# Performance work log

Hardware: AMD Instinct MI355X
Metric: run time of the kernel (lower is better)

The kernel has to match this reference:

```python
import jax, jax.numpy as jnp
import numpy as np

B = 16384
STATE = 524   # state_dim / output_size
IENC = 256    # INet output dim
ZD = 32       # z_dim
H = 256       # expert hidden size
E = 5         # num_experts
HG = 256      # gating hidden size
IN1 = STATE + IENC + ZD   # 812, PredictionNet layer-1 input
IN2 = H + ZD              # 288, layers 2/3 input


def _uni(k, shape):
    # matches PredictionNet.init_params glorot-style uniform bound
    bound = float(np.sqrt(6.0 / (shape[-2] * shape[-1])))
    return jax.random.uniform(k, shape, jnp.float32, -bound, bound)


def setup_inputs() -> dict:
    key = jax.random.key(0)
    ks = jax.random.split(key, 12)
    d = {}
    d['z'] = jax.random.normal(ks[0], (B, ZD), jnp.float32)
    d['p_prev'] = jax.random.normal(ks[1], (B, STATE), jnp.float32)
    d['I'] = jax.random.normal(ks[2], (B, 2048), jnp.float32)
    # gating network: (state+z) -> HG -> HG//2 -> E
    d['gw1'] = _uni(ks[3], (STATE + ZD, HG)); d['gb1'] = jnp.zeros((HG,), jnp.float32)
    d['gw2'] = _uni(ks[4], (HG, HG // 2));    d['gb2'] = jnp.zeros((HG // 2,), jnp.float32)
    d['gw3'] = _uni(ks[5], (HG // 2, E));     d['gb3'] = jnp.zeros((E,), jnp.float32)
    # INet: 2048 -> 256 -> 256 -> 256
    d['iw1'] = _uni(ks[6], (2048, IENC)); d['ib1'] = jnp.zeros((IENC,), jnp.float32)
    d['iw2'] = _uni(ks[7], (IENC, IENC)); d['ib2'] = jnp.zeros((IENC,), jnp.float32)
    d['iw3'] = _uni(ks[8], (IENC, IENC)); d['ib3'] = jnp.zeros((IENC,), jnp.float32)
    # expert weights [E, in, out], biases [E, out]
    d['w_l1'] = _uni(ks[9], (E, IN1, H));     d['b_l1'] = jnp.zeros((E, H), jnp.float32)
    d['w_l2'] = _uni(ks[10], (E, IN2, H));    d['b_l2'] = jnp.zeros((E, H), jnp.float32)
    d['w_l3'] = _uni(ks[11], (E, IN2, STATE)); d['b_l3'] = jnp.zeros((E, STATE), jnp.float32)
    return d


def reference(z, p_prev, I, gw1, gb1, gw2, gb2, gw3, gb3,
              iw1, ib1, iw2, ib2, iw3, ib3,
              w_l1, b_l1, w_l2, b_l2, w_l3, b_l3):
    elu = jax.nn.elu
    # gating network -> softmax blending coefficients omega [B, E]
    g = elu(jnp.concatenate([z, p_prev], axis=1) @ gw1 + gb1)
    g = elu(g @ gw2 + gb2)
    omega = jax.nn.softmax(g @ gw3 + gb3, axis=-1)
    # interaction encoder
    Ienc = elu(elu(elu(I @ iw1 + ib1) @ iw2 + ib2) @ iw3 + ib3)
    x = jnp.concatenate([p_prev, Ienc], axis=1)  # [B, STATE+IENC]

    def moe_linear(h, W, b):
        # same math as sum_e omega_e * (h @ W_e) + omega @ b, without
        # materializing per-sample blended [B, in, out] weights
        per_expert = jnp.einsum('bi,eio->beo', h, W)
        return jnp.einsum('be,beo->bo', omega, per_expert) + omega @ b

    h0 = jnp.concatenate([z, x], axis=1)          # [B, 812]
    h1 = elu(moe_linear(h0, w_l1, b_l1))          # [B, 256]
    h2 = elu(moe_linear(jnp.concatenate([z, h1], axis=1), w_l2, b_l2))
    h3 = moe_linear(jnp.concatenate([z, h2], axis=1), w_l3, b_l3)  # [B, 524]
    return h3
```

## Files before the change

### kernel.cpp

```cpp
#include <hip/hip_runtime.h>
#include <hip/hip_bf16.h>
#include <cstdint>
#include <cstddef>


#define BATCH 16384

typedef __attribute__((ext_vector_type(8))) short short8;
typedef __attribute__((ext_vector_type(4))) float f32x4;
typedef unsigned short u16;
typedef unsigned int u32;

typedef __attribute__((address_space(3))) void lds_t;
typedef __attribute__((address_space(1))) void gmem_t;

__device__ __forceinline__ void gload16(const u16* g, u16* l) {
  __builtin_amdgcn_global_load_lds((gmem_t*)(u16*)g, (lds_t*)l, 16, 0, 0);
}

__device__ __forceinline__ float bf2f(u16 u) {
  union { float f; u32 i; } v; v.i = ((u32)u) << 16; return v.f;
}
__device__ __forceinline__ u16 f2bf(float f) {
  union { float f; u32 i; } v; v.f = f;
  u32 x = v.i;
  return (u16)((x + 0x7fffu + ((x >> 16) & 1u)) >> 16);
}
__device__ __forceinline__ u16 load_bf(const void* p, long i, int f32) {
  return f32 ? f2bf(((const float*)p)[i]) : ((const u16*)p)[i];
}
__device__ __forceinline__ float elu_f(float x) { return x > 0.f ? x : expm1f(x); }

__device__ __forceinline__ int swz(int row, int q) { return q ^ ((row >> 1) & 3); }

__global__ __launch_bounds__(256) void detect_dtype(const u32* __restrict__ zr,
                                                    int* __restrict__ flag)
{
  __shared__ int cnt;
  if (threadIdx.x == 0) cnt = 0;
  __syncthreads();
  u32 w = zr[threadIdx.x];
  int e = (w >> 7) & 0xFF;
  if (e >= 112 && e <= 142) atomicAdd(&cnt, 1);
  __syncthreads();
  if (threadIdx.x == 0) *flag = (cnt < 128) ? 1 : 0;
}

__global__ __launch_bounds__(256) void prep_kernel(
    const void* __restrict__ z, const void* __restrict__ p,
    const int* __restrict__ flagp,
    u16* __restrict__ h0, u16* __restrict__ h1c, u16* __restrict__ h2c,
    const void* ib1, const void* ib2, const void* ib3,
    const void* gb1, const void* gb2, const void* gb3,
    const void* gw3, const void* bl1, const void* bl2, const void* bl3,
    u16* __restrict__ smallc)
{
  const int f32 = *flagp;
  const int b = blockIdx.y;
  const int c = blockIdx.x * 256 + threadIdx.x;
  if (blockIdx.y == 0 && blockIdx.x == 0) {
    for (long j = threadIdx.x; j < 7100; j += 256) {
      u16 v;
      if      (j < 256)  v = load_bf(ib1, j,        f32);
      else if (j < 512)  v = load_bf(ib2, j - 256,  f32);
      else if (j < 768)  v = load_bf(ib3, j - 512,  f32);
      else if (j < 1024) v = load_bf(gb1, j - 768,  f32);
      else if (j < 1152) v = load_bf(gb2, j - 1024, f32);
      else if (j < 1280) v = (j - 1152 < 5) ? load_bf(gb3, j - 1152, f32) : (u16)0;
      else if (j < 1920) v = load_bf(gw3, j - 1280, f32);
      else if (j < 3200) v = load_bf(bl1, j - 1920, f32);
      else if (j < 4480) v = load_bf(bl2, j - 3200, f32);
      else               v = load_bf(bl3, j - 4480, f32);
      smallc[j] = v;
    }
  }
  if (c >= 832) return;
  const long i = (long)b * 832 + c;
  if (c < 32) {
    u16 v = load_bf(z, (long)b * 32 + c, f32);
    h0[i] = v;
    h1c[(long)b * 288 + c] = v;
    h2c[(long)b * 288 + c] = v;
  } else if (c < 556) {
    h0[i] = load_bf(p, (long)b * 524 + (c - 32), f32);
  } else if (c >= 812) {
    h0[i] = 0;
  }
}

__global__ __launch_bounds__(256) void convert_I(
    const void* __restrict__ I, const int* __restrict__ flagp,
    u16* __restrict__ out)
{
  const int f32 = *flagp;
  const long total8 = (long)BATCH * 2048 / 8;
  const long stride = (long)gridDim.x * blockDim.x;
  for (long t = (long)blockIdx.x * blockDim.x + threadIdx.x; t < total8; t += stride) {
    if (f32) {
      const float4* src = (const float4*)I;
      float4 a = src[t * 2], b = src[t * 2 + 1];
      union { u16 r[8]; uint4 v; } u;
      u.r[0] = f2bf(a.x); u.r[1] = f2bf(a.y); u.r[2] = f2bf(a.z); u.r[3] = f2bf(a.w);
      u.r[4] = f2bf(b.x); u.r[5] = f2bf(b.y); u.r[6] = f2bf(b.z); u.r[7] = f2bf(b.w);
      *(uint4*)(out + t * 8) = u.v;
    } else {
      *(uint4*)(out + t * 8) = ((const uint4*)I)[t];
    }
  }
}

struct TPSeg { long end; int K, N, Kp, Np; };

__global__ __launch_bounds__(256) void transpose_all(
    const int* __restrict__ flagp,
    const void* s0, const void* s1, const void* s2, const void* s3,
    const void* s4, const void* s5, const void* s6, const void* s7,
    u16* d0, u16* d1, u16* d2, u16* d3, u16* d4, u16* d5, u16* d6, u16* d7)
{
  const TPSeg seg[8] = {
    {  524288, 2048, 256, 2048, 256 },
    {  589824,  256, 256,  256, 256 },
    {  655360,  256, 256,  256, 256 },
    {  802816,  556, 256,  576, 256 },
    {  835584,  256, 128,  256, 128 },
    { 1900544,  812, 256,  832, 256 },
    { 2269184,  288, 256,  288, 256 },
    { 3098624,  288, 524,  288, 576 },
  };
  const void* const srcs[8] = { s0, s1, s2, s3, s4, s5, s6, s7 };
  u16* const dsts[8] = { d0, d1, d2, d3, d4, d5, d6, d7 };
  const int f32 = *flagp;
  const long total = 3098624;
  const long stride = (long)gridDim.x * blockDim.x;
  for (long i = (long)blockIdx.x * blockDim.x + threadIdx.x; i < total; i += stride) {
    int s = 0;
    long base = 0;
    while (i >= seg[s].end) { base = seg[s].end; ++s; }
    const long j = i - base;
    const int Kp = seg[s].Kp, Np = seg[s].Np, K = seg[s].K, N = seg[s].N;
    const int k = (int)(j % Kp);
    const long t = j / Kp;
    const int n = (int)(t % Np);
    const int e = (int)(t / Np);
    u16 v = 0;
    if (k < K && n < N) v = load_bf(srcs[s], (long)e * K * N + (long)k * N + n, f32);
    dsts[s][j] = v;
  }
}

template<bool ELU>
__global__ __launch_bounds__(256) void gemm128(
    const u16* __restrict__ A, int lda,
    const u16* __restrict__ Wt, int ldw,
    const u16* __restrict__ bias,
    u16* __restrict__ C, int ldc, int col_off, int K)
{
  __shared__ __align__(16) u16 sA[128 * 32];
  __shared__ __align__(16) u16 sB[128 * 32];

  const int tid  = threadIdx.x;
  const int bm   = blockIdx.x, bn = blockIdx.y;
  const int lane = tid & 63, wave = tid >> 6;
  const int wm = (wave & 1) * 64, wn = (wave >> 1) * 64;
  const int lrow = lane & 15, lq = lane >> 4;

  const int srow0 = 32 * wave + (lane >> 2);
  const int sq    = (lane & 3) ^ ((lane >> 3) & 3);
  const u16* Ag = A  + (size_t)(bm * 128 + srow0) * lda + sq * 8;
  const u16* Wg = Wt + (size_t)(bn * 128 + srow0) * ldw + sq * 8;
  u16* lA = sA + wave * 1024;
  u16* lB = sB + wave * 1024;

  f32x4 acc[4][4] = {};

  for (int k0 = 0; k0 < K; k0 += 32) {
    __syncthreads();
    gload16(Ag + k0, lA);
    gload16(Ag + (size_t)16 * lda + k0, lA + 512);
    gload16(Wg + k0, lB);
    gload16(Wg + (size_t)16 * ldw + k0, lB + 512);
    __syncthreads();

    short8 a[4], b[4];
#pragma unroll
    for (int i = 0; i < 4; ++i) {
      const int r = wm + i * 16 + lrow;
      a[i] = *(const short8*)(sA + r * 32 + swz(r, lq) * 8);
    }
#pragma unroll
    for (int i = 0; i < 4; ++i) {
      const int r = wn + i * 16 + lrow;
      b[i] = *(const short8*)(sB + r * 32 + swz(r, lq) * 8);
    }

#pragma unroll
    for (int mi = 0; mi < 4; ++mi)
#pragma unroll
      for (int ni = 0; ni < 4; ++ni)
        acc[mi][ni] = __builtin_amdgcn_mfma_f32_16x16x32_bf16(a[mi], b[ni], acc[mi][ni], 0, 0, 0);
  }

#pragma unroll
  for (int ni = 0; ni < 4; ++ni) {
    const int col = bn * 128 + wn + ni * 16 + lrow;
    const float bv = bf2f(bias[col]);
#pragma unroll
    for (int mi = 0; mi < 4; ++mi) {
#pragma unroll
      for (int r = 0; r < 4; ++r) {
        const int row = bm * 128 + wm + mi * 16 + lq * 4 + r;
        float v = acc[mi][ni][r] + bv;
        if (ELU) v = elu_f(v);
        C[(size_t)row * ldc + col_off + col] = f2bf(v);
      }
    }
  }
}

__global__ __launch_bounds__(256) void gating3_kernel(
    const u16* __restrict__ g2, const u16* __restrict__ gw3c,
    const u16* __restrict__ gb3c, float* __restrict__ omega)
{
  const int wid  = (blockIdx.x << 2) + (threadIdx.x >> 6);
  const int lane = threadIdx.x & 63;
  const u32 gp = *(const u32*)(g2 + (size_t)wid * 128 + lane * 2);
  const float x0 = bf2f((u16)(gp & 0xffffu));
  const float x1 = bf2f((u16)(gp >> 16));
  float acc[5];
#pragma unroll
  for (int e = 0; e < 5; ++e)
    acc[e] = x0 * bf2f(gw3c[(lane * 2) * 5 + e]) + x1 * bf2f(gw3c[(lane * 2 + 1) * 5 + e]);
#pragma unroll
  for (int off = 1; off < 64; off <<= 1) {
#pragma unroll
    for (int e = 0; e < 5; ++e) acc[e] += __shfl_xor(acc[e], off);
  }
  if (lane == 0) {
    float t[5], m = -1e30f;
#pragma unroll
    for (int e = 0; e < 5; ++e) { t[e] = acc[e] + bf2f(gb3c[e]); m = fmaxf(m, t[e]); }
    float s = 0.f;
#pragma unroll
    for (int e = 0; e < 5; ++e) { t[e] = expf(t[e] - m); s += t[e]; }
    const float inv = 1.f / s;
#pragma unroll
    for (int e = 0; e < 5; ++e) omega[(size_t)wid * 5 + e] = t[e] * inv;
  }
}

template<bool ELU>
__global__ __launch_bounds__(256, 2) void moe_gemm(
    const u16* __restrict__ A, int lda,
    const u16* __restrict__ Wt, int ldw, long wstride_e,
    const u16* __restrict__ bias, int bias_n,
    const float* __restrict__ omega,
    void* __restrict__ C, int ldc, int col_off, int n_store, int K,
    const int* __restrict__ flagp, int is_final)
{
  __shared__ __align__(16) u16 sA[128 * 32];
  __shared__ __align__(16) u16 sW[5][64 * 32];
  __shared__ float som[128 * 5];
  __shared__ float sbias[5][64];

  const int tid  = threadIdx.x;
  const int bm   = blockIdx.x, bn = blockIdx.y;
  const int lane = tid & 63, wave = tid >> 6;
  const int wm = (wave & 1) * 64, wn = (wave >> 1) * 32;
  const int lrow = lane & 15, lq = lane >> 4;
  const int f32out = is_final ? *flagp : 0;

  for (int t = tid; t < 960; t += 256) {
    if (t < 640) {
      som[t] = omega[(size_t)(bm * 128) * 5 + t];
    } else {
      const int j = t - 640;
      const int e = j >> 6, c = j & 63;
      const int col = bn * 64 + c;
      sbias[e][c] = (col < bias_n) ? bf2f(bias[(size_t)e * bias_n + col]) : 0.f;
    }
  }

  const int sq = (lane & 3) ^ ((lane >> 3) & 3);
  const int srowA = 32 * wave + (lane >> 2);
  const int srowW = 16 * wave + (lane >> 2);
  const u16* Ag = A  + (size_t)(bm * 128 + srowA) * lda + sq * 8;
  const u16* Wg = Wt + (size_t)(bn * 64 + srowW) * ldw + sq * 8;
  u16* lA = sA + wave * 1024;
  const int lWoff = wave * 512;

  f32x4 acc[5][4][2] = {};

  for (int k0 = 0; k0 < K; k0 += 32) {
    __syncthreads();
    gload16(Ag + k0, lA);
    gload16(Ag + (size_t)16 * lda + k0, lA + 512);
#pragma unroll
    for (int e = 0; e < 5; ++e)
      gload16(Wg + e * wstride_e + k0, sW[e] + lWoff);
    __syncthreads();

    short8 a[4];
#pragma unroll
    for (int i = 0; i < 4; ++i) {
      const int r = wm + i * 16 + lrow;
      a[i] = *(const short8*)(sA + r * 32 + swz(r, lq) * 8);
    }
    const int rb0 = wn + lrow, rb1 = rb0 + 16;
    const int ob0 = rb0 * 32 + swz(rb0, lq) * 8;
    const int ob1 = rb1 * 32 + swz(rb1, lq) * 8;
#pragma unroll
    for (int e = 0; e < 5; ++e) {
      short8 b0 = *(const short8*)(sW[e] + ob0);
      short8 b1 = *(const short8*)(sW[e] + ob1);
#pragma unroll
      for (int mi = 0; mi < 4; ++mi) {
        acc[e][mi][0] = __builtin_amdgcn_mfma_f32_16x16x32_bf16(a[mi], b0, acc[e][mi][0], 0, 0, 0);
        acc[e][mi][1] = __builtin_amdgcn_mfma_f32_16x16x32_bf16(a[mi], b1, acc[e][mi][1], 0, 0, 0);
      }
    }
  }

#pragma unroll
  for (int mi = 0; mi < 4; ++mi) {
#pragma unroll
    for (int r = 0; r < 4; ++r) {
      const int rl = wm + mi * 16 + lq * 4 + r;
      const int row = bm * 128 + rl;
      float om[5];
#pragma unroll
      for (int e = 0; e < 5; ++e) om[e] = som[rl * 5 + e];
#pragma unroll
      for (int ni = 0; ni < 2; ++ni) {
        const int c = wn + ni * 16 + lrow;
        const int col = bn * 64 + c;
        if (col < n_store) {
          float v = 0.f;
#pragma unroll
          for (int e = 0; e < 5; ++e) v += om[e] * (acc[e][mi][ni][r] + sbias[e][c]);
          if (ELU) v = elu_f(v);
          const size_t idx = (size_t)row * ldc + col_off + col;
          if (f32out) ((float*)C)[idx] = v;
          else        ((u16*)C)[idx]   = f2bf(v);
        }
      }
    }
  }
}

extern "C" void kernel_launch(void* const* d_in, const int* in_sizes, int n_in,
                              void* d_out, int out_size, void* d_ws, size_t ws_size,
                              hipStream_t stream)
{
  const void* z    = d_in[0];
  const void* pprev= d_in[1];
  const void* I    = d_in[2];
  const void* gw1  = d_in[3];
  const void* gb1  = d_in[4];
  const void* gw2  = d_in[5];
  const void* gb2  = d_in[6];
  const void* gw3  = d_in[7];
  const void* gb3  = d_in[8];
  const void* iw1  = d_in[9];
  const void* ib1  = d_in[10];
  const void* iw2  = d_in[11];
  const void* ib2  = d_in[12];
  const void* iw3  = d_in[13];
  const void* ib3  = d_in[14];
  const void* wl1  = d_in[15];
  const void* bl1  = d_in[16];
  const void* wl2  = d_in[17];
  const void* bl2  = d_in[18];
  const void* wl3  = d_in[19];
  const void* bl3  = d_in[20];

  char* base = (char*)d_ws;
  size_t off = 0;
  auto alloc = [&](size_t bytes) -> void* {
    void* p = base + off;
    off = (off + bytes + 255) & ~(size_t)255;
    return p;
  };

  const size_t B = BATCH;
  int* flagp   = (int*)alloc(256);
  u16* h0      = (u16*)alloc(B * 832 * 2);
  u16* h1c     = (u16*)alloc(B * 288 * 2);
  u16* h2c     = (u16*)alloc(B * 288 * 2);
  u16* i1      = (u16*)alloc(B * 256 * 2);
  u16* i2      = (u16*)alloc(B * 256 * 2);
  float* omega = (float*)alloc(B * 5 * 4);
  u16* Ibf     = (u16*)alloc(B * 2048 * 2);
  u16* smallc  = (u16*)alloc(7100 * 2);
  u16* iw1t = (u16*)alloc((size_t)256 * 2048 * 2);
  u16* iw2t = (u16*)alloc((size_t)256 * 256 * 2);
  u16* iw3t = (u16*)alloc((size_t)256 * 256 * 2);
  u16* gw1t = (u16*)alloc((size_t)256 * 576 * 2);
  u16* gw2t = (u16*)alloc((size_t)128 * 256 * 2);
  u16* wl1t = (u16*)alloc((size_t)5 * 256 * 832 * 2);
  u16* wl2t = (u16*)alloc((size_t)5 * 256 * 288 * 2);
  u16* wl3t = (u16*)alloc((size_t)5 * 576 * 288 * 2);
  u16* g1 = i1;
  u16* g2 = i2;
  (void)in_sizes; (void)n_in; (void)out_size; (void)ws_size;

  u16* ib1c = smallc + 0,   *ib2c = smallc + 256, *ib3c = smallc + 512;
  u16* gb1c = smallc + 768, *gb2c = smallc + 1024, *gb3c = smallc + 1152;
  u16* gw3c = smallc + 1280;
  u16* bl1c = smallc + 1920, *bl2c = smallc + 3200, *bl3c = smallc + 4480;

  detect_dtype<<<1, 256, 0, stream>>>((const u32*)z, flagp);
  prep_kernel<<<dim3(4, BATCH), 256, 0, stream>>>(z, pprev, flagp, h0, h1c, h2c,
      ib1, ib2, ib3, gb1, gb2, gb3, gw3, bl1, bl2, bl3, smallc);
  convert_I<<<4096, 256, 0, stream>>>(I, flagp, Ibf);
  transpose_all<<<3072, 256, 0, stream>>>(flagp,
      iw1, iw2, iw3, gw1, gw2, wl1, wl2, wl3,
      iw1t, iw2t, iw3t, gw1t, gw2t, wl1t, wl2t, wl3t);

  gemm128<true><<<dim3(BATCH/128, 2), 256, 0, stream>>>(Ibf, 2048, iw1t, 2048, ib1c, i1, 256, 0,   2048);
  gemm128<true><<<dim3(BATCH/128, 2), 256, 0, stream>>>(i1,  256,  iw2t, 256,  ib2c, i2, 256, 0,   256);
  gemm128<true><<<dim3(BATCH/128, 2), 256, 0, stream>>>(i2,  256,  iw3t, 256,  ib3c, h0, 832, 556, 256);

  gemm128<true><<<dim3(BATCH/128, 2), 256, 0, stream>>>(h0, 832, gw1t, 576, gb1c, g1, 256, 0, 576);
  gemm128<true><<<dim3(BATCH/128, 1), 256, 0, stream>>>(g1, 256, gw2t, 256, gb2c, g2, 128, 0, 256);
  gating3_kernel<<<BATCH/4, 256, 0, stream>>>(g2, gw3c, gb3c, omega);

  moe_gemm<true><<<dim3(BATCH/128, 4), 256, 0, stream>>>(
      h0, 832, wl1t, 832, (long)256 * 832, bl1c, 256, omega, h1c, 288, 32, 256, 832, flagp, 0);
  moe_gemm<true><<<dim3(BATCH/128, 4), 256, 0, stream>>>(
      h1c, 288, wl2t, 288, (long)256 * 288, bl2c, 256, omega, h2c, 288, 32, 256, 288, flagp, 0);
  moe_gemm<false><<<dim3(BATCH/128, 9), 256, 0, stream>>>(
      h2c, 288, wl3t, 288, (long)576 * 288, bl3c, 524, omega, d_out, 524, 0, 524, 288, flagp, 1);
}
```

Before: 589.6 us.

## Fuse I fp32->bf16 conversion into GEMM and double-buffer LDS tiles

Removes the separate convert_I pass and its bf16 staging buffer: the first INet GEMM now reads fp32 I directly, converts in registers and writes bf16 into LDS. Both the dense GEMM and the MoE GEMM gain double-buffered LDS tiles, so the next K-slice is issued before the MFMAs on the current one, with one barrier per iteration instead of two. This avoids a full write and re-read of the 64 MB-scale I tensor and hides load latency, at the cost of twice the LDS per block and a register-path conversion that is synchronous with the MFMA loop.

```diff
diff --git a/kernel.cpp b/kernel.cpp
--- a/kernel.cpp
+++ b/kernel.cpp
@@ -30,6 +30,15 @@
   return f32 ? f2bf(((const float*)p)[i]) : ((const u16*)p)[i];
 }
 __device__ __forceinline__ float elu_f(float x) { return x > 0.f ? x : expm1f(x); }
+
+__device__ __forceinline__ uint4 cvt8(uint4 a, uint4 b) {
+  const float* fa = (const float*)&a;
+  const float* fb = (const float*)&b;
+  union { u16 r[8]; uint4 v; } u;
+  u.r[0] = f2bf(fa[0]); u.r[1] = f2bf(fa[1]); u.r[2] = f2bf(fa[2]); u.r[3] = f2bf(fa[3]);
+  u.r[4] = f2bf(fb[0]); u.r[5] = f2bf(fb[1]); u.r[6] = f2bf(fb[2]); u.r[7] = f2bf(fb[3]);
+  return u.v;
+}
 
 __device__ __forceinline__ int swz(int row, int q) { return q ^ ((row >> 1) & 3); }
 
@@ -85,27 +94,6 @@
     h0[i] = load_bf(p, (long)b * 524 + (c - 32), f32);
   } else if (c >= 812) {
     h0[i] = 0;
-  }
-}
-
-__global__ __launch_bounds__(256) void convert_I(
-    const void* __restrict__ I, const int* __restrict__ flagp,
-    u16* __restrict__ out)
-{
-  const int f32 = *flagp;
-  const long total8 = (long)BATCH * 2048 / 8;
-  const long stride = (long)gridDim.x * blockDim.x;
-  for (long t = (long)blockIdx.x * blockDim.x + threadIdx.x; t < total8; t += stride) {
-    if (f32) {
-      const float4* src = (const float4*)I;
-      float4 a = src[t * 2], b = src[t * 2 + 1];
-      union { u16 r[8]; uint4 v; } u;
-      u.r[0] = f2bf(a.x); u.r[1] = f2bf(a.y); u.r[2] = f2bf(a.z); u.r[3] = f2bf(a.w);
-      u.r[4] = f2bf(b.x); u.r[5] = f2bf(b.y); u.r[6] = f2bf(b.z); u.r[7] = f2bf(b.w);
-      *(uint4*)(out + t * 8) = u.v;
-    } else {
-      *(uint4*)(out + t * 8) = ((const uint4*)I)[t];
-    }
   }
 }
 
@@ -148,56 +136,89 @@
   }
 }
 
-template<bool ELU>
-__global__ __launch_bounds__(256) void gemm128(
-    const u16* __restrict__ A, int lda,
+template<bool ELU, bool ACONV>
+__global__ __launch_bounds__(256, 2) void gemm128(
+    const void* __restrict__ Av, int lda,
     const u16* __restrict__ Wt, int ldw,
     const u16* __restrict__ bias,
-    u16* __restrict__ C, int ldc, int col_off, int K)
-{
-  __shared__ __align__(16) u16 sA[128 * 32];
-  __shared__ __align__(16) u16 sB[128 * 32];
+    u16* __restrict__ C, int ldc, int col_off, int K,
+    const int* __restrict__ flagp)
+{
+  __shared__ __align__(16) u16 sA[2][128 * 32];
+  __shared__ __align__(16) u16 sB[2][128 * 32];
 
   const int tid  = threadIdx.x;
   const int bm   = blockIdx.x, bn = blockIdx.y;
   const int lane = tid & 63, wave = tid >> 6;
   const int wm = (wave & 1) * 64, wn = (wave >> 1) * 64;
   const int lrow = lane & 15, lq = lane >> 4;
+  const int f32 = ACONV ? *flagp : 0;
 
   const int srow0 = 32 * wave + (lane >> 2);
   const int sq    = (lane & 3) ^ ((lane >> 3) & 3);
-  const u16* Ag = A  + (size_t)(bm * 128 + srow0) * lda + sq * 8;
+  const u16*   A16 = (const u16*)Av   + (size_t)(bm * 128 + srow0) * lda + sq * 8;
+  const float* A32 = (const float*)Av + (size_t)(bm * 128 + srow0) * lda + sq * 8;
   const u16* Wg = Wt + (size_t)(bn * 128 + srow0) * ldw + sq * 8;
-  u16* lA = sA + wave * 1024;
-  u16* lB = sB + wave * 1024;
+  const int lofs  = wave * 1024;
+  const int lslot = wave * 1024 + lane * 8;
+
+  if (ACONV && f32) {
+    uint4 p0 = *(const uint4*)(A32);
+    uint4 p1 = *(const uint4*)(A32 + 4);
+    uint4 p2 = *(const uint4*)(A32 + (size_t)16 * lda);
+    uint4 p3 = *(const uint4*)(A32 + (size_t)16 * lda + 4);
+    *(uint4*)(sA[0] + lslot)       = cvt8(p0, p1);
+    *(uint4*)(sA[0] + lslot + 512) = cvt8(p2, p3);
+  } else {
+    gload16(A16, sA[0] + lofs);
+    gload16(A16 + (size_t)16 * lda, sA[0] + lofs + 512);
+  }
+  gload16(Wg, sB[0] + lofs);
+  gload16(Wg + (size_t)16 * ldw, sB[0] + lofs + 512);
 
   f32x4 acc[4][4] = {};
-
-  for (int k0 = 0; k0 < K; k0 += 32) {
+  int pb = 0;
+  for (int k0 = 0; k0 < K; k0 += 32, pb ^= 1) {
     __syncthreads();
-    gload16(Ag + k0, lA);
-    gload16(Ag + (size_t)16 * lda + k0, lA + 512);
-    gload16(Wg + k0, lB);
-    gload16(Wg + (size_t)16 * ldw + k0, lB + 512);
-    __syncthreads();
+
+    const int k1 = k0 + 32;
+    const bool pf = k1 < K;
+    uint4 q0, q1, q2, q3;
+    if (pf) {
+      if (ACONV && f32) {
+        q0 = *(const uint4*)(A32 + k1);
+        q1 = *(const uint4*)(A32 + k1 + 4);
+        q2 = *(const uint4*)(A32 + (size_t)16 * lda + k1);
+        q3 = *(const uint4*)(A32 + (size_t)16 * lda + k1 + 4);
+      } else {
+        gload16(A16 + k1, sA[pb ^ 1] + lofs);
+        gload16(A16 + (size_t)16 * lda + k1, sA[pb ^ 1] + lofs + 512);
+      }
+      gload16(Wg + k1, sB[pb ^ 1] + lofs);
+      gload16(Wg + (size_t)16 * ldw + k1, sB[pb ^ 1] + lofs + 512);
+    }
 
     short8 a[4], b[4];
 #pragma unroll
     for (int i = 0; i < 4; ++i) {
       const int r = wm + i * 16 + lrow;
-      a[i] = *(const short8*)(sA + r * 32 + swz(r, lq) * 8);
+      a[i] = *(const short8*)(sA[pb] + r * 32 + swz(r, lq) * 8);
     }
 #pragma unroll
     for (int i = 0; i < 4; ++i) {
       const int r = wn + i * 16 + lrow;
-      b[i] = *(const short8*)(sB + r * 32 + swz(r, lq) * 8);
-    }
-
+      b[i] = *(const short8*)(sB[pb] + r * 32 + swz(r, lq) * 8);
+    }
 #pragma unroll
     for (int mi = 0; mi < 4; ++mi)
 #pragma unroll
       for (int ni = 0; ni < 4; ++ni)
         acc[mi][ni] = __builtin_amdgcn_mfma_f32_16x16x32_bf16(a[mi], b[ni], acc[mi][ni], 0, 0, 0);
+
+    if (pf && ACONV && f32) {
+      *(uint4*)(sA[pb ^ 1] + lslot)       = cvt8(q0, q1);
+      *(uint4*)(sA[pb ^ 1] + lslot + 512) = cvt8(q2, q3);
+    }
   }
 
 #pragma unroll
@@ -257,8 +278,8 @@
     void* __restrict__ C, int ldc, int col_off, int n_store, int K,
     const int* __restrict__ flagp, int is_final)
 {
-  __shared__ __align__(16) u16 sA[128 * 32];
-  __shared__ __align__(16) u16 sW[5][64 * 32];
+  __shared__ __align__(16) u16 sA[2][128 * 32];
+  __shared__ __align__(16) u16 sW[2][5][64 * 32];
   __shared__ float som[128 * 5];
   __shared__ float sbias[5][64];
 
@@ -268,6 +289,20 @@
   const int wm = (wave & 1) * 64, wn = (wave >> 1) * 32;
   const int lrow = lane & 15, lq = lane >> 4;
   const int f32out = is_final ? *flagp : 0;
+
+  const int sq = (lane & 3) ^ ((lane >> 3) & 3);
+  const int srowA = 32 * wave + (lane >> 2);
+  const int srowW = 16 * wave + (lane >> 2);
+  const u16* Ag = A  + (size_t)(bm * 128 + srowA) * lda + sq * 8;
+  const u16* Wg = Wt + (size_t)(bn * 64 + srowW) * ldw + sq * 8;
+  const int lofsA = wave * 1024;
+  const int lofsW = wave * 512;
+
+  gload16(Ag, sA[0] + lofsA);
+  gload16(Ag + (size_t)16 * lda, sA[0] + lofsA + 512);
+#pragma unroll
+  for (int e = 0; e < 5; ++e)
+    gload16(Wg + e * wstride_e, sW[0][e] + lofsW);
 
   for (int t = tid; t < 960; t += 256) {
     if (t < 640) {
@@ -280,38 +315,33 @@
     }
   }
 
-  const int sq = (lane & 3) ^ ((lane >> 3) & 3);
-  const int srowA = 32 * wave + (lane >> 2);
-  const int srowW = 16 * wave + (lane >> 2);
-  const u16* Ag = A  + (size_t)(bm * 128 + srowA) * lda + sq * 8;
-  const u16* Wg = Wt + (size_t)(bn * 64 + srowW) * ldw + sq * 8;
-  u16* lA = sA + wave * 1024;
-  const int lWoff = wave * 512;
-
   f32x4 acc[5][4][2] = {};
-
-  for (int k0 = 0; k0 < K; k0 += 32) {
+  int pb = 0;
+  for (int k0 = 0; k0 < K; k0 += 32, pb ^= 1) {
     __syncthreads();
-    gload16(Ag + k0, lA);
-    gload16(Ag + (size_t)16 * lda + k0, lA + 512);
-#pragma unroll
-    for (int e = 0; e < 5; ++e)
-      gload16(Wg + e * wstride_e + k0, sW[e] + lWoff);
-    __syncthreads();
+
+    const int k1 = k0 + 32;
+    if (k1 < K) {
+      gload16(Ag + k1, sA[pb ^ 1] + lofsA);
+      gload16(Ag + (size_t)16 * lda + k1, sA[pb ^ 1] + lofsA + 512);
+#pragma unroll
+      for (int e = 0; e < 5; ++e)
+        gload16(Wg + e * wstride_e + k1, sW[pb ^ 1][e] + lofsW);
+    }
 
     short8 a[4];
 #pragma unroll
     for (int i = 0; i < 4; ++i) {
       const int r = wm + i * 16 + lrow;
-      a[i] = *(const short8*)(sA + r * 32 + swz(r, lq) * 8);
+      a[i] = *(const short8*)(sA[pb] + r * 32 + swz(r, lq) * 8);
     }
     const int rb0 = wn + lrow, rb1 = rb0 + 16;
     const int ob0 = rb0 * 32 + swz(rb0, lq) * 8;
     const int ob1 = rb1 * 32 + swz(rb1, lq) * 8;
 #pragma unroll
     for (int e = 0; e < 5; ++e) {
-      short8 b0 = *(const short8*)(sW[e] + ob0);
-      short8 b1 = *(const short8*)(sW[e] + ob1);
+      short8 b0 = *(const short8*)(sW[pb][e] + ob0);
+      short8 b1 = *(const short8*)(sW[pb][e] + ob1);
 #pragma unroll
       for (int mi = 0; mi < 4; ++mi) {
         acc[e][mi][0] = __builtin_amdgcn_mfma_f32_16x16x32_bf16(a[mi], b0, acc[e][mi][0], 0, 0, 0);
@@ -389,7 +419,6 @@
   u16* i1      = (u16*)alloc(B * 256 * 2);
   u16* i2      = (u16*)alloc(B * 256 * 2);
   float* omega = (float*)alloc(B * 5 * 4);
-  u16* Ibf     = (u16*)alloc(B * 2048 * 2);
   u16* smallc  = (u16*)alloc(7100 * 2);
   u16* iw1t = (u16*)alloc((size_t)256 * 2048 * 2);
   u16* iw2t = (u16*)alloc((size_t)256 * 256 * 2);
@@ -411,17 +440,16 @@
   detect_dtype<<<1, 256, 0, stream>>>((const u32*)z, flagp);
   prep_kernel<<<dim3(4, BATCH), 256, 0, stream>>>(z, pprev, flagp, h0, h1c, h2c,
       ib1, ib2, ib3, gb1, gb2, gb3, gw3, bl1, bl2, bl3, smallc);
-  convert_I<<<4096, 256, 0, stream>>>(I, flagp, Ibf);
   transpose_all<<<3072, 256, 0, stream>>>(flagp,
       iw1, iw2, iw3, gw1, gw2, wl1, wl2, wl3,
       iw1t, iw2t, iw3t, gw1t, gw2t, wl1t, wl2t, wl3t);
 
-  gemm128<true><<<dim3(BATCH/128, 2), 256, 0, stream>>>(Ibf, 2048, iw1t, 2048, ib1c, i1, 256, 0,   2048);
-  gemm128<true><<<dim3(BATCH/128, 2), 256, 0, stream>>>(i1,  256,  iw2t, 256,  ib2c, i2, 256, 0,   256);
-  gemm128<true><<<dim3(BATCH/128, 2), 256, 0, stream>>>(i2,  256,  iw3t, 256,  ib3c, h0, 832, 556, 256);
-
-  gemm128<true><<<dim3(BATCH/128, 2), 256, 0, stream>>>(h0, 832, gw1t, 576, gb1c, g1, 256, 0, 576);
-  gemm128<true><<<dim3(BATCH/128, 1), 256, 0, stream>>>(g1, 256, gw2t, 256, gb2c, g2, 128, 0, 256);
+  gemm128<true, true ><<<dim3(BATCH/128, 2), 256, 0, stream>>>(I,  2048, iw1t, 2048, ib1c, i1, 256, 0,   2048, flagp);
+  gemm128<true, false><<<dim3(BATCH/128, 2), 256, 0, stream>>>(i1, 256,  iw2t, 256,  ib2c, i2, 256, 0,   256,  flagp);
+  gemm128<true, false><<<dim3(BATCH/128, 2), 256, 0, stream>>>(i2, 256,  iw3t, 256,  ib3c, h0, 832, 556, 256,  flagp);
+
+  gemm128<true, false><<<dim3(BATCH/128, 2), 256, 0, stream>>>(h0, 832, gw1t, 576, gb1c, g1, 256, 0, 576, flagp);
+  gemm128<true, false><<<dim3(BATCH/128, 1), 256, 0, stream>>>(g1, 256, gw2t, 256, gb2c, g2, 128, 0, 256, flagp);
   gating3_kernel<<<BATCH/4, 256, 0, stream>>>(g2, gw3c, gb3c, omega);
 
   moe_gemm<true><<<dim3(BATCH/128, 4), 256, 0, stream>>>(
```

Measured after the change: 590.3 us. No clear change (+0.1%).
